# Kernel optimization log

Measured on AMD Instinct MI355X. Metric: run time of the kernel, lower is better.

## Reference

```python
import jax, jax.numpy as jnp
import numpy as np
import math

B, C, HW = 4, 256, 32          # batch, seq_len (=channels), spatial side
D_MODEL = HW * HW              # 1024
OUT_C = 32 * 32                # 1024
D_STATE = 16
EXPAND = 2
D_INNER = EXPAND * D_MODEL     # 2048
DT_RANK = math.ceil(D_MODEL / 16)  # 64
D_CONV = 4


def setup_inputs() -> dict:
    key = jax.random.key(0)
    ks = jax.random.split(key, 12)
    s = 0.02
    x1 = jax.random.normal(ks[0], (B, C, HW, HW), dtype=jnp.float32)
    in_proj_w = jax.random.normal(ks[1], (2 * D_INNER, D_MODEL), dtype=jnp.float32) * s
    conv_w = jax.random.normal(ks[2], (D_INNER, 1, D_CONV), dtype=jnp.float32) * s
    conv_b = jnp.zeros((D_INNER,), dtype=jnp.float32)
    x_proj_w = jax.random.normal(ks[3], (DT_RANK + 2 * D_STATE, D_INNER), dtype=jnp.float32) * s
    dt_proj_w = jax.random.normal(ks[4], (D_INNER, DT_RANK), dtype=jnp.float32) * s
    dt_proj_b = jnp.zeros((D_INNER,), dtype=jnp.float32)
    A_log = jnp.log(jnp.broadcast_to(jnp.arange(1, D_STATE + 1, dtype=jnp.float32), (D_INNER, D_STATE)))
    D = jnp.ones((D_INNER,), dtype=jnp.float32)
    out_proj_w = jax.random.normal(ks[5], (OUT_C, D_INNER), dtype=jnp.float32) * s
    ln_w = jnp.ones((OUT_C,), dtype=jnp.float32)
    ln_b = jnp.zeros((OUT_C,), dtype=jnp.float32)
    return {"x1": x1, "in_proj_w": in_proj_w, "conv_w": conv_w, "conv_b": conv_b,
            "x_proj_w": x_proj_w, "dt_proj_w": dt_proj_w, "dt_proj_b": dt_proj_b,
            "A_log": A_log, "D": D, "out_proj_w": out_proj_w, "ln_w": ln_w, "ln_b": ln_b}


def _mamba_forward(x, in_proj_w, conv_w, conv_b, x_proj_w, dt_proj_w, dt_proj_b, A_log, D, out_proj_w):
    # x: (B, L, d_model)
    xz = jnp.einsum('bld,ed->ble', x, in_proj_w)            # (B,L,2*d_inner)
    xs, res = jnp.split(xz, 2, axis=-1)                     # each (B,L,d_inner)
    # depthwise causal conv1d, padding=d_conv-1 then truncate to L (== left pad)
    xs_c = jnp.transpose(xs, (0, 2, 1))                     # (B,d_inner,L)
    xs_c = jax.lax.conv_general_dilated(
        xs_c, conv_w, window_strides=(1,), padding=[(D_CONV - 1, 0)],
        dimension_numbers=('NCH', 'OIH', 'NCH'), feature_group_count=D_INNER)
    xs_c = xs_c + conv_b[None, :, None]
    xs = jax.nn.silu(jnp.transpose(xs_c, (0, 2, 1)))        # (B,L,d_inner)
    # input-dependent SSM parameters
    x_dbl = jnp.einsum('bld,ed->ble', xs, x_proj_w)         # (B,L,dt_rank+2N)
    dt, Bm, Cm = jnp.split(x_dbl, [DT_RANK, DT_RANK + D_STATE], axis=-1)
    delta = jax.nn.softplus(jnp.einsum('blr,dr->bld', dt, dt_proj_w) + dt_proj_b)  # (B,L,d_inner)
    A = -jnp.exp(A_log)                                     # (d_inner, N)
    deltaA = jnp.exp(delta[..., None] * A)                  # (B,L,d_inner,N)
    deltaB_u = delta[..., None] * Bm[:, :, None, :] * xs[..., None]  # (B,L,d_inner,N)

    def step(h, inp):
        dA, dBu, Ct = inp                                   # (B,d,N),(B,d,N),(B,N)
        h = dA * h + dBu
        y = jnp.einsum('bdn,bn->bd', h, Ct)
        return h, y

    h0 = jnp.zeros((deltaA.shape[0], D_INNER, D_STATE), dtype=deltaA.dtype)
    _, ys = jax.lax.scan(step, h0, (jnp.transpose(deltaA, (1, 0, 2, 3)),
                                    jnp.transpose(deltaB_u, (1, 0, 2, 3)),
                                    jnp.transpose(Cm, (1, 0, 2))))
    y = jnp.transpose(ys, (1, 0, 2))                        # (B,L,d_inner)
    y = y + D * xs
    y = y * jax.nn.silu(res)
    return jnp.einsum('bld,od->blo', y, out_proj_w)         # (B,L,out_c)


def reference(x1, in_proj_w, conv_w, conv_b, x_proj_w, dt_proj_w, dt_proj_b,
              A_log, D, out_proj_w, ln_w, ln_b):
    b, c, h, w = x1.shape
    x = x1.reshape(b, c, h * w)                             # (B, L=c, d_model)
    y = _mamba_forward(x, in_proj_w, conv_w, conv_b, x_proj_w, dt_proj_w,
                       dt_proj_b, A_log, D, out_proj_w)
    mu = jnp.mean(y, axis=-1, keepdims=True)
    var = jnp.var(y, axis=-1, keepdims=True)
    y = (y - mu) * jax.lax.rsqrt(var + 1e-5) * ln_w + ln_b
    return y.reshape(b, c, 32, 32)
```

## Files before the change

kernel.cpp:

```cpp
#include <hip/hip_runtime.h>
#include <hip/hip_bf16.h>
#include <math.h>

#define BATCH 4
#define SEQL 256
#define DMODEL 1024
#define DINNER 2048
#define DSTATE 16
#define DTRANK 64
#define OUTC 1024
#define NROWS (BATCH * SEQL)
#define NCHUNK 4
#define CH 64

typedef __attribute__((ext_vector_type(8))) short bf16x8;
typedef __attribute__((ext_vector_type(4))) float f32x4;

__global__ __launch_bounds__(256) void gemm_mfma(const __hip_bfloat16* __restrict__ A,
                                                 const __hip_bfloat16* __restrict__ B,
                                                 float* __restrict__ C,
                                                 int M, int N, int K,
                                                 int lda, int ldb) {
    __shared__ __hip_bfloat16 As[4][128 * 32];
    __shared__ __hip_bfloat16 Bs[4][128 * 32];
    const int t  = threadIdx.x;
    const int w  = t >> 6;
    const int ln = t & 63;
    const int wm = w >> 1, wn = w & 1;
    const int q  = ln >> 4, lr = ln & 15;
    const int m0 = blockIdx.y * 128;
    const int n0 = blockIdx.x * 128;
    const int Kpart = K / gridDim.z;
    const int kbase = blockIdx.z * Kpart;

    f32x4 acc[4][4] = {};

    const __hip_bfloat16* Ag = A + (size_t)m0 * lda + kbase;
    const __hip_bfloat16* Bg = B + (size_t)n0 * ldb + kbase;

    auto stage = [&](int k0, int buf) {
        #pragma unroll
        for (int i = 0; i < 2; ++i) {
            const int c = (i * 4 + w) * 64 + ln;
            const int r = c >> 2, col = (c & 3) * 8;
            __builtin_amdgcn_global_load_lds(
                (const __attribute__((address_space(1))) void*)(Ag + (size_t)r * lda + k0 + col),
                (__attribute__((address_space(3))) void*)(As[buf] + (i * 4 + w) * 64 * 8),
                16, 0, 0);
            __builtin_amdgcn_global_load_lds(
                (const __attribute__((address_space(1))) void*)(Bg + (size_t)r * ldb + k0 + col),
                (__attribute__((address_space(3))) void*)(Bs[buf] + (i * 4 + w) * 64 * 8),
                16, 0, 0);
        }
    };

    const int nk = Kpart / 32;
    for (int s = 0; s < 3 && s < nk; ++s) stage(s * 32, s);

    for (int kk = 0; kk < nk; ++kk) {
        const int last = (kk + 2 < nk - 1) ? (kk + 2) : (nk - 1);
        const int nf = last - kk;
        if (nf >= 2)      asm volatile("s_waitcnt vmcnt(8)" ::: "memory");
        else if (nf == 1) asm volatile("s_waitcnt vmcnt(4)" ::: "memory");
        else              asm volatile("s_waitcnt vmcnt(0)" ::: "memory");
        __builtin_amdgcn_s_barrier();
        if (kk + 3 < nk) stage((kk + 3) * 32, (kk + 3) & 3);

        const int buf = kk & 3;
        bf16x8 af[4], bfr[4];
        #pragma unroll
        for (int i = 0; i < 4; ++i)
            af[i] = *(const bf16x8*)(As[buf] + (wm * 64 + i * 16 + lr) * 32 + q * 8);
        #pragma unroll
        for (int j = 0; j < 4; ++j)
            bfr[j] = *(const bf16x8*)(Bs[buf] + (wn * 64 + j * 16 + lr) * 32 + q * 8);
        #pragma unroll
        for (int i = 0; i < 4; ++i)
            #pragma unroll
            for (int j = 0; j < 4; ++j)
                acc[i][j] = __builtin_amdgcn_mfma_f32_16x16x32_bf16(af[i], bfr[j], acc[i][j], 0, 0, 0);
    }
    float* Cz = C + (size_t)blockIdx.z * M * N;
    #pragma unroll
    for (int i = 0; i < 4; ++i) {
        const int mrow = m0 + wm * 64 + i * 16 + q * 4;
        #pragma unroll
        for (int j = 0; j < 4; ++j) {
            const int ncol = n0 + wn * 64 + j * 16 + lr;
            #pragma unroll
            for (int r = 0; r < 4; ++r)
                Cz[(size_t)(mrow + r) * N + ncol] = acc[i][j][r];
        }
    }
}

__global__ __launch_bounds__(256) void gemm_dtsp(const __hip_bfloat16* __restrict__ A,
                                                 const __hip_bfloat16* __restrict__ B,
                                                 const float* __restrict__ bd,
                                                 float* __restrict__ delta) {
    __shared__ __hip_bfloat16 As[2][128 * 32];
    __shared__ __hip_bfloat16 Bs[2][128 * 32];
    const int t  = threadIdx.x;
    const int w  = t >> 6;
    const int ln = t & 63;
    const int wm = w >> 1, wn = w & 1;
    const int q  = ln >> 4, lr = ln & 15;
    const int m0 = blockIdx.y * 128;
    const int n0 = blockIdx.x * 128;
    const int lda = 128, ldb = 64, N = 2048;

    f32x4 acc[4][4] = {};
    const __hip_bfloat16* Ag = A + (size_t)m0 * lda;
    const __hip_bfloat16* Bg = B + (size_t)n0 * ldb;

    auto stage = [&](int k0, int buf) {
        #pragma unroll
        for (int i = 0; i < 2; ++i) {
            const int c = (i * 4 + w) * 64 + ln;
            const int r = c >> 2, col = (c & 3) * 8;
            __builtin_amdgcn_global_load_lds(
                (const __attribute__((address_space(1))) void*)(Ag + (size_t)r * lda + k0 + col),
                (__attribute__((address_space(3))) void*)(As[buf] + (i * 4 + w) * 64 * 8),
                16, 0, 0);
            __builtin_amdgcn_global_load_lds(
                (const __attribute__((address_space(1))) void*)(Bg + (size_t)r * ldb + k0 + col),
                (__attribute__((address_space(3))) void*)(Bs[buf] + (i * 4 + w) * 64 * 8),
                16, 0, 0);
        }
    };

    stage(0, 0);
    stage(32, 1);
    #pragma unroll
    for (int kk = 0; kk < 2; ++kk) {
        if (kk == 0) asm volatile("s_waitcnt vmcnt(4)" ::: "memory");
        else         asm volatile("s_waitcnt vmcnt(0)" ::: "memory");
        __builtin_amdgcn_s_barrier();
        bf16x8 af[4], bfr[4];
        #pragma unroll
        for (int i = 0; i < 4; ++i)
            af[i] = *(const bf16x8*)(As[kk] + (wm * 64 + i * 16 + lr) * 32 + q * 8);
        #pragma unroll
        for (int j = 0; j < 4; ++j)
            bfr[j] = *(const bf16x8*)(Bs[kk] + (wn * 64 + j * 16 + lr) * 32 + q * 8);
        #pragma unroll
        for (int i = 0; i < 4; ++i)
            #pragma unroll
            for (int j = 0; j < 4; ++j)
                acc[i][j] = __builtin_amdgcn_mfma_f32_16x16x32_bf16(af[i], bfr[j], acc[i][j], 0, 0, 0);
    }
    #pragma unroll
    for (int i = 0; i < 4; ++i) {
        const int mrow = m0 + wm * 64 + i * 16 + q * 4;
        #pragma unroll
        for (int j = 0; j < 4; ++j) {
            const int ncol = n0 + wn * 64 + j * 16 + lr;
            const float bias = bd[ncol];
            #pragma unroll
            for (int r = 0; r < 4; ++r) {
                float v = acc[i][j][r] + bias;
                float sp = (v > 20.f) ? v : log1pf(__expf(v));
                delta[(size_t)(mrow + r) * N + ncol] = sp;
            }
        }
    }
}

__global__ void xdbl_reduce_kernel(const float* __restrict__ part,
                                   float* __restrict__ xdbl,
                                   __hip_bfloat16* __restrict__ xdblb) {
    const int i = blockIdx.x * 256 + threadIdx.x;
    float s = 0.f;
    #pragma unroll
    for (int z = 0; z < 8; ++z) s += part[(size_t)z * (1024 * 128) + i];
    xdbl[i] = s;
    xdblb[i] = __float2bfloat16(s);
}

#define R0 (1024 * 1024)
#define R1 (R0 + 4096 * 1024)
#define R2 (R1 + 2048 * 1024)
#define R3 (R2 + 128 * 2048)
#define R4 (R3 + 2048 * 64)
__global__ void cast_all_kernel(const float* __restrict__ x1,
                                const float* __restrict__ w_in,
                                const float* __restrict__ w_out,
                                const float* __restrict__ w_xp,
                                const float* __restrict__ w_dt,
                                __hip_bfloat16* __restrict__ xa,
                                __hip_bfloat16* __restrict__ wb1,
                                __hip_bfloat16* __restrict__ wob,
                                __hip_bfloat16* __restrict__ wpb,
                                __hip_bfloat16* __restrict__ wdb) {
    int i = blockIdx.x * 256 + threadIdx.x;
    if (i < R0) {
        xa[i] = __float2bfloat16(x1[i]);
    } else if (i < R1) {
        int j = i - R0; wb1[j] = __float2bfloat16(w_in[j]);
    } else if (i < R2) {
        int j = i - R1; wob[j] = __float2bfloat16(w_out[j]);
    } else if (i < R3) {
        int j = i - R2; int e = j >> 11;
        wpb[j] = __float2bfloat16(e < 96 ? w_xp[j] : 0.f);
    } else if (i < R4) {
        int j = i - R3; wdb[j] = __float2bfloat16(w_dt[j]);
    }
}

__global__ void conv_silu_kernel(const float* __restrict__ xz,
                                 const float* __restrict__ conv_w,
                                 const float* __restrict__ conv_b,
                                 float* __restrict__ xs,
                                 __hip_bfloat16* __restrict__ xsb) {
    int idx = blockIdx.x * blockDim.x + threadIdx.x;
    int d = idx & (DINNER - 1);
    int l = (idx >> 11) & (SEQL - 1);
    int b = idx >> 19;
    const float w0 = conv_w[d * 4 + 0];
    const float w1 = conv_w[d * 4 + 1];
    const float w2 = conv_w[d * 4 + 2];
    const float w3 = conv_w[d * 4 + 3];
    float acc = conv_b[d];
    const size_t base = (size_t)(b * SEQL) * (2 * DINNER) + d;
    if (l >= 3) acc += w0 * xz[base + (size_t)(l - 3) * (2 * DINNER)];
    if (l >= 2) acc += w1 * xz[base + (size_t)(l - 2) * (2 * DINNER)];
    if (l >= 1) acc += w2 * xz[base + (size_t)(l - 1) * (2 * DINNER)];
    acc += w3 * xz[base + (size_t)l * (2 * DINNER)];
    float v = acc / (1.f + __expf(-acc));
    xs[idx] = v;
    xsb[idx] = __float2bfloat16(v);
}

__device__ __forceinline__ float row_reduce16(float x) {
    x += __int_as_float(__builtin_amdgcn_update_dpp(0, __float_as_int(x), 0x128, 0xF, 0xF, true));
    x += __int_as_float(__builtin_amdgcn_update_dpp(0, __float_as_int(x), 0x124, 0xF, 0xF, true));
    x += __int_as_float(__builtin_amdgcn_update_dpp(0, __float_as_int(x), 0x122, 0xF, 0xF, true));
    x += __int_as_float(__builtin_amdgcn_update_dpp(0, __float_as_int(x), 0x121, 0xF, 0xF, true));
    return x;
}

__global__ __launch_bounds__(256) void scan_carry_kernel(const float* __restrict__ delta,
                                                         const float* __restrict__ xs,
                                                         const float* __restrict__ xdbl,
                                                         const float* __restrict__ A_log,
                                                         float* __restrict__ carryL,
                                                         float* __restrict__ carryP) {
    __shared__ float sDU[CH][16][2];
    __shared__ float sB[CH][16];
    const int b = blockIdx.y, c = blockIdx.z, dg = blockIdx.x;
    const int t = threadIdx.x;
    const int dl = t >> 4, n = t & 15;
    const int d = dg * 16 + dl;
    const float a = -__expf(A_log[d * DSTATE + n]);
    const int srow = t >> 4, scol = t & 15;
    const int sd = dg * 16 + scol;
    const int rowbase = b * SEQL + c * CH;
    #pragma unroll
    for (int i = 0; i < 4; ++i) {
        const int row = rowbase + i * 16 + srow;
        const float dv = delta[(size_t)row * DINNER + sd];
        const float xv = xs[(size_t)row * DINNER + sd];
        sDU[i * 16 + srow][scol][0] = dv;
        sDU[i * 16 + srow][scol][1] = dv * xv;
        sB[i * 16 + srow][scol] = xdbl[row * 128 + 64 + scol];
    }
    __syncthreads();
    float h = 0.f, P = 1.f;
    #pragma unroll 16
    for (int l = 0; l < CH; ++l) {
        const float e = __expf(sDU[l][dl][0] * a);
        h = e * h + sDU[l][dl][1] * sB[l][n];
        P *= e;
    }
    const size_t ci = (((size_t)(b * NCHUNK + c)) * DINNER + d) * DSTATE + n;
    carryL[ci] = h;
    carryP[ci] = P;
}

__global__ __launch_bounds__(256) void scan_apply_kernel(const float* __restrict__ delta,
                                                         const float* __restrict__ xs,
                                                         const float* __restrict__ xdbl,
                                                         const float* __restrict__ xz,
                                                         const float* __restrict__ A_log,
                                                         const float* __restrict__ Dp,
                                                         const float* __restrict__ carryL,
                                                         const float* __restrict__ carryP,
                                                         __hip_bfloat16* __restrict__ ybb) {
    __shared__ float sDU[CH][16][2];
    __shared__ float sBC[CH][16][2];
    __shared__ float sGW[CH][16][2];
    const int b = blockIdx.y, c = blockIdx.z, dg = blockIdx.x;
    const int t = threadIdx.x;
    const int dl = t >> 4, n = t & 15;
    const int d = dg * 16 + dl;
    const float a = -__expf(A_log[d * DSTATE + n]);
    const int srow = t >> 4, scol = t & 15;
    const int sd = dg * 16 + scol;
    const float Dstage = Dp[sd];
    const int rowbase = b * SEQL + c * CH;
    #pragma unroll
    for (int i = 0; i < 4; ++i) {
        const int row = rowbase + i * 16 + srow;
        const float dv = delta[(size_t)row * DINNER + sd];
        const float xv = xs[(size_t)row * DINNER + sd];
        const float r  = xz[(size_t)row * (2 * DINNER) + DINNER + sd];
        const float g = r / (1.f + __expf(-r));
        const int lr_ = i * 16 + srow;
        sDU[lr_][scol][0] = dv;
        sDU[lr_][scol][1] = dv * xv;
        sGW[lr_][scol][0] = g;
        sGW[lr_][scol][1] = Dstage * xv * g;
        sBC[lr_][scol][0] = xdbl[row * 128 + 64 + scol];
        sBC[lr_][scol][1] = xdbl[row * 128 + 80 + scol];
    }
    __syncthreads();
    float h = 0.f;
    for (int j = 0; j < c; ++j) {
        const size_t ci = (((size_t)(b * NCHUNK + j)) * DINNER + d) * DSTATE + n;
        h = carryP[ci] * h + carryL[ci];
    }
    #pragma unroll 16
    for (int l = 0; l < CH; ++l) {
        const float e = __expf(sDU[l][dl][0] * a);
        h = e * h + sDU[l][dl][1] * sBC[l][n][0];
        float p = row_reduce16(h * sBC[l][n][1]);
        if (n == 0) {
            const float y = p * sGW[l][dl][0] + sGW[l][dl][1];
            ybb[(size_t)(rowbase + l) * DINNER + d] = __float2bfloat16(y);
        }
    }
}

__global__ __launch_bounds__(256) void ln_kernel(const float* __restrict__ opart,
                                                 const float* __restrict__ lw,
                                                 const float* __restrict__ lb,
                                                 float* __restrict__ out) {
    __shared__ float red[8];
    const int row = blockIdx.x;
    const int t = threadIdx.x;
    float v[4];
    float s = 0.f, s2 = 0.f;
    #pragma unroll
    for (int i = 0; i < 4; ++i) {
        const int c = t + 256 * i;
        float acc = 0.f;
        #pragma unroll
        for (int z = 0; z < 4; ++z)
            acc += opart[(size_t)z * (1024 * 1024) + (size_t)row * OUTC + c];
        v[i] = acc;
        s += acc;
        s2 += acc * acc;
    }
    #pragma unroll
    for (int o = 32; o; o >>= 1) {
        s += __shfl_down(s, o);
        s2 += __shfl_down(s2, o);
    }
    const int wid = t >> 6;
    if ((t & 63) == 0) { red[wid] = s; red[4 + wid] = s2; }
    __syncthreads();
    if (t == 0) {
        float ts = red[0] + red[1] + red[2] + red[3];
        float ts2 = red[4] + red[5] + red[6] + red[7];
        float mu = ts * (1.f / OUTC);
        float var = ts2 * (1.f / OUTC) - mu * mu;
        red[0] = mu;
        red[1] = rsqrtf(var + 1e-5f);
    }
    __syncthreads();
    const float mu = red[0], rs = red[1];
    #pragma unroll
    for (int i = 0; i < 4; ++i) {
        const int c = t + 256 * i;
        out[(size_t)row * OUTC + c] = (v[i] - mu) * rs * lw[c] + lb[c];
    }
}

extern "C" void kernel_launch(void* const* d_in, const int* in_sizes, int n_in,
                              void* d_out, int out_size, void* d_ws, size_t ws_size,
                              hipStream_t stream) {
    const float* x1        = (const float*)d_in[0];
    const float* in_proj_w = (const float*)d_in[1];
    const float* conv_w    = (const float*)d_in[2];
    const float* conv_b    = (const float*)d_in[3];
    const float* x_proj_w  = (const float*)d_in[4];
    const float* dt_proj_w = (const float*)d_in[5];
    const float* dt_proj_b = (const float*)d_in[6];
    const float* A_log     = (const float*)d_in[7];
    const float* Dp        = (const float*)d_in[8];
    const float* out_proj_w= (const float*)d_in[9];
    const float* ln_w      = (const float*)d_in[10];
    const float* ln_b      = (const float*)d_in[11];
    float* out = (float*)d_out;

    char* p = (char*)d_ws;
    __hip_bfloat16* xa    = (__hip_bfloat16*)p; p += (size_t)1024 * 1024 * 2;
    __hip_bfloat16* wb1   = (__hip_bfloat16*)p; p += (size_t)4096 * 1024 * 2;
    __hip_bfloat16* wpb   = (__hip_bfloat16*)p; p += (size_t)128 * 2048 * 2;
    __hip_bfloat16* wob   = (__hip_bfloat16*)p; p += (size_t)1024 * 2048 * 2;
    __hip_bfloat16* wdb   = (__hip_bfloat16*)p; p += (size_t)2048 * 64 * 2;
    __hip_bfloat16* xsb   = (__hip_bfloat16*)p; p += (size_t)1024 * 2048 * 2;
    __hip_bfloat16* ybb   = (__hip_bfloat16*)p; p += (size_t)1024 * 2048 * 2;
    __hip_bfloat16* xdblb = (__hip_bfloat16*)p; p += (size_t)1024 * 128 * 2;
    float* xz    = (float*)p; p += (size_t)1024 * 4096 * 4;
    float* xs    = (float*)p; p += (size_t)1024 * 2048 * 4;
    float* xdbl  = (float*)p; p += (size_t)1024 * 128 * 4;
    float* xpart = (float*)p; p += (size_t)8 * 1024 * 128 * 4;
    float* delta = (float*)p; p += (size_t)1024 * 2048 * 4;
    float* carryL = (float*)p; p += (size_t)BATCH * NCHUNK * DINNER * DSTATE * 4;
    float* carryP = (float*)p; p += (size_t)BATCH * NCHUNK * DINNER * DSTATE * 4;
    float* opart = xz;

    cast_all_kernel<<<(R4 + 255) / 256, 256, 0, stream>>>(x1, in_proj_w, out_proj_w,
                                                          x_proj_w, dt_proj_w,
                                                          xa, wb1, wob, wpb, wdb);
    gemm_mfma<<<dim3(32, 8, 1), 256, 0, stream>>>(xa, wb1, xz,
                                                  NROWS, 2 * DINNER, DMODEL, DMODEL, DMODEL);
    conv_silu_kernel<<<(NROWS * DINNER) / 256, 256, 0, stream>>>(xz, conv_w, conv_b, xs, xsb);
    gemm_mfma<<<dim3(1, 8, 8), 256, 0, stream>>>(xsb, wpb, xpart,
                                                 NROWS, 128, DINNER, DINNER, DINNER);
    xdbl_reduce_kernel<<<(1024 * 128) / 256, 256, 0, stream>>>(xpart, xdbl, xdblb);
    gemm_dtsp<<<dim3(16, 8), 256, 0, stream>>>(xdblb, wdb, dt_proj_b, delta);
    scan_carry_kernel<<<dim3(DINNER / 16, BATCH, NCHUNK), 256, 0, stream>>>(
        delta, xs, xdbl, A_log, carryL, carryP);
    scan_apply_kernel<<<dim3(DINNER / 16, BATCH, NCHUNK), 256, 0, stream>>>(
        delta, xs, xdbl, xz, A_log, Dp, carryL, carryP, ybb);
    gemm_mfma<<<dim3(8, 8, 4), 256, 0, stream>>>(ybb, wob, opart,
                                                 NROWS, OUTC, DINNER, DINNER, DINNER);
    ln_kernel<<<NROWS, 256, 0, stream>>>(opart, ln_w, ln_b, out);
}
```

Before: 220.0 us.

## Fuse all stages into one persistent cooperative kernel with grid syncs

```diff
diff --git a/kernel.cpp b/kernel.cpp
--- a/kernel.cpp
+++ b/kernel.cpp
@@ -1,40 +1,57 @@
 #include <hip/hip_runtime.h>
+#include <hip/hip_cooperative_groups.h>
 #include <hip/hip_bf16.h>
 #include <math.h>
+
+namespace cg = cooperative_groups;
 
 #define BATCH 4
 #define SEQL 256
 #define DMODEL 1024
 #define DINNER 2048
 #define DSTATE 16
-#define DTRANK 64
 #define OUTC 1024
 #define NROWS (BATCH * SEQL)
 #define NCHUNK 4
 #define CH 64
+#define NBLK 256
+#define XPZ 32
 
 typedef __attribute__((ext_vector_type(8))) short bf16x8;
 typedef __attribute__((ext_vector_type(4))) float f32x4;
 
-__global__ __launch_bounds__(256) void gemm_mfma(const __hip_bfloat16* __restrict__ A,
-                                                 const __hip_bfloat16* __restrict__ B,
-                                                 float* __restrict__ C,
-                                                 int M, int N, int K,
-                                                 int lda, int ldb) {
-    __shared__ __hip_bfloat16 As[4][128 * 32];
-    __shared__ __hip_bfloat16 Bs[4][128 * 32];
+struct MParams {
+    const float *x1, *w_in, *conv_w, *conv_b, *w_xp, *w_dt, *dt_b, *A_log, *Dp, *w_out, *ln_w, *ln_b;
+    float *out;
+    __hip_bfloat16 *xa, *wb1, *wpb, *wob, *wdb, *xsb, *ybb, *xdblb;
+    float *xz, *xs, *xdbl, *xpart, *delta, *carryL, *carryP, *opart;
+};
+
+__device__ __forceinline__ float row_reduce16(float x) {
+    x += __int_as_float(__builtin_amdgcn_update_dpp(0, __float_as_int(x), 0x128, 0xF, 0xF, true));
+    x += __int_as_float(__builtin_amdgcn_update_dpp(0, __float_as_int(x), 0x124, 0xF, 0xF, true));
+    x += __int_as_float(__builtin_amdgcn_update_dpp(0, __float_as_int(x), 0x122, 0xF, 0xF, true));
+    x += __int_as_float(__builtin_amdgcn_update_dpp(0, __float_as_int(x), 0x121, 0xF, 0xF, true));
+    return x;
+}
+
+template <bool DTSP>
+__device__ __forceinline__ void gemm_tile(const __hip_bfloat16* __restrict__ A,
+                                          const __hip_bfloat16* __restrict__ B,
+                                          float* __restrict__ Cz,
+                                          const int N, const int lda, const int ldb,
+                                          const int m0, const int n0,
+                                          const int kbase, const int Kpart,
+                                          const float* __restrict__ bd,
+                                          __hip_bfloat16* __restrict__ As,
+                                          __hip_bfloat16* __restrict__ Bs) {
     const int t  = threadIdx.x;
     const int w  = t >> 6;
     const int ln = t & 63;
     const int wm = w >> 1, wn = w & 1;
     const int q  = ln >> 4, lr = ln & 15;
-    const int m0 = blockIdx.y * 128;
-    const int n0 = blockIdx.x * 128;
-    const int Kpart = K / gridDim.z;
-    const int kbase = blockIdx.z * Kpart;
 
     f32x4 acc[4][4] = {};
-
     const __hip_bfloat16* Ag = A + (size_t)m0 * lda + kbase;
     const __hip_bfloat16* Bg = B + (size_t)n0 * ldb + kbase;
 
@@ -45,11 +62,11 @@
             const int r = c >> 2, col = (c & 3) * 8;
             __builtin_amdgcn_global_load_lds(
                 (const __attribute__((address_space(1))) void*)(Ag + (size_t)r * lda + k0 + col),
-                (__attribute__((address_space(3))) void*)(As[buf] + (i * 4 + w) * 64 * 8),
+                (__attribute__((address_space(3))) void*)(As + buf * 4096 + (i * 4 + w) * 512),
                 16, 0, 0);
             __builtin_amdgcn_global_load_lds(
                 (const __attribute__((address_space(1))) void*)(Bg + (size_t)r * ldb + k0 + col),
-                (__attribute__((address_space(3))) void*)(Bs[buf] + (i * 4 + w) * 64 * 8),
+                (__attribute__((address_space(3))) void*)(Bs + buf * 4096 + (i * 4 + w) * 512),
                 16, 0, 0);
         }
     };
@@ -66,115 +83,42 @@
         __builtin_amdgcn_s_barrier();
         if (kk + 3 < nk) stage((kk + 3) * 32, (kk + 3) & 3);
 
-        const int buf = kk & 3;
+        const __hip_bfloat16* Ab = As + (kk & 3) * 4096;
+        const __hip_bfloat16* Bb = Bs + (kk & 3) * 4096;
         bf16x8 af[4], bfr[4];
         #pragma unroll
         for (int i = 0; i < 4; ++i)
-            af[i] = *(const bf16x8*)(As[buf] + (wm * 64 + i * 16 + lr) * 32 + q * 8);
+            af[i] = *(const bf16x8*)(Ab + (wm * 64 + i * 16 + lr) * 32 + q * 8);
         #pragma unroll
         for (int j = 0; j < 4; ++j)
-            bfr[j] = *(const bf16x8*)(Bs[buf] + (wn * 64 + j * 16 + lr) * 32 + q * 8);
+            bfr[j] = *(const bf16x8*)(Bb + (wn * 64 + j * 16 + lr) * 32 + q * 8);
         #pragma unroll
         for (int i = 0; i < 4; ++i)
             #pragma unroll
             for (int j = 0; j < 4; ++j)
                 acc[i][j] = __builtin_amdgcn_mfma_f32_16x16x32_bf16(af[i], bfr[j], acc[i][j], 0, 0, 0);
     }
-    float* Cz = C + (size_t)blockIdx.z * M * N;
     #pragma unroll
     for (int i = 0; i < 4; ++i) {
         const int mrow = m0 + wm * 64 + i * 16 + q * 4;
         #pragma unroll
         for (int j = 0; j < 4; ++j) {
             const int ncol = n0 + wn * 64 + j * 16 + lr;
-            #pragma unroll
-            for (int r = 0; r < 4; ++r)
-                Cz[(size_t)(mrow + r) * N + ncol] = acc[i][j][r];
-        }
-    }
-}
-
-__global__ __launch_bounds__(256) void gemm_dtsp(const __hip_bfloat16* __restrict__ A,
-                                                 const __hip_bfloat16* __restrict__ B,
-                                                 const float* __restrict__ bd,
-                                                 float* __restrict__ delta) {
-    __shared__ __hip_bfloat16 As[2][128 * 32];
-    __shared__ __hip_bfloat16 Bs[2][128 * 32];
-    const int t  = threadIdx.x;
-    const int w  = t >> 6;
-    const int ln = t & 63;
-    const int wm = w >> 1, wn = w & 1;
-    const int q  = ln >> 4, lr = ln & 15;
-    const int m0 = blockIdx.y * 128;
-    const int n0 = blockIdx.x * 128;
-    const int lda = 128, ldb = 64, N = 2048;
-
-    f32x4 acc[4][4] = {};
-    const __hip_bfloat16* Ag = A + (size_t)m0 * lda;
-    const __hip_bfloat16* Bg = B + (size_t)n0 * ldb;
-
-    auto stage = [&](int k0, int buf) {
-        #pragma unroll
-        for (int i = 0; i < 2; ++i) {
-            const int c = (i * 4 + w) * 64 + ln;
-            const int r = c >> 2, col = (c & 3) * 8;
-            __builtin_amdgcn_global_load_lds(
-                (const __attribute__((address_space(1))) void*)(Ag + (size_t)r * lda + k0 + col),
-                (__attribute__((address_space(3))) void*)(As[buf] + (i * 4 + w) * 64 * 8),
-                16, 0, 0);
-            __builtin_amdgcn_global_load_lds(
-                (const __attribute__((address_space(1))) void*)(Bg + (size_t)r * ldb + k0 + col),
-                (__attribute__((address_space(3))) void*)(Bs[buf] + (i * 4 + w) * 64 * 8),
-                16, 0, 0);
-        }
-    };
-
-    stage(0, 0);
-    stage(32, 1);
-    #pragma unroll
-    for (int kk = 0; kk < 2; ++kk) {
-        if (kk == 0) asm volatile("s_waitcnt vmcnt(4)" ::: "memory");
-        else         asm volatile("s_waitcnt vmcnt(0)" ::: "memory");
-        __builtin_amdgcn_s_barrier();
-        bf16x8 af[4], bfr[4];
-        #pragma unroll
-        for (int i = 0; i < 4; ++i)
-            af[i] = *(const bf16x8*)(As[kk] + (wm * 64 + i * 16 + lr) * 32 + q * 8);
-        #pragma unroll
-        for (int j = 0; j < 4; ++j)
-            bfr[j] = *(const bf16x8*)(Bs[kk] + (wn * 64 + j * 16 + lr) * 32 + q * 8);
-        #pragma unroll
-        for (int i = 0; i < 4; ++i)
-            #pragma unroll
-            for (int j = 0; j < 4; ++j)
-                acc[i][j] = __builtin_amdgcn_mfma_f32_16x16x32_bf16(af[i], bfr[j], acc[i][j], 0, 0, 0);
-    }
-    #pragma unroll
-    for (int i = 0; i < 4; ++i) {
-        const int mrow = m0 + wm * 64 + i * 16 + q * 4;
-        #pragma unroll
-        for (int j = 0; j < 4; ++j) {
-            const int ncol = n0 + wn * 64 + j * 16 + lr;
-            const float bias = bd[ncol];
-            #pragma unroll
-            for (int r = 0; r < 4; ++r) {
-                float v = acc[i][j][r] + bias;
-                float sp = (v > 20.f) ? v : log1pf(__expf(v));
-                delta[(size_t)(mrow + r) * N + ncol] = sp;
-            }
-        }
-    }
-}
-
-__global__ void xdbl_reduce_kernel(const float* __restrict__ part,
-                                   float* __restrict__ xdbl,
-                                   __hip_bfloat16* __restrict__ xdblb) {
-    const int i = blockIdx.x * 256 + threadIdx.x;
-    float s = 0.f;
-    #pragma unroll
-    for (int z = 0; z < 8; ++z) s += part[(size_t)z * (1024 * 128) + i];
-    xdbl[i] = s;
-    xdblb[i] = __float2bfloat16(s);
+            if (DTSP) {
+                const float bias = bd[ncol];
+                #pragma unroll
+                for (int r = 0; r < 4; ++r) {
+                    float v = acc[i][j][r] + bias;
+                    float sp = (v > 20.f) ? v : log1pf(__expf(v));
+                    Cz[(size_t)(mrow + r) * N + ncol] = sp;
+                }
+            } else {
+                #pragma unroll
+                for (int r = 0; r < 4; ++r)
+                    Cz[(size_t)(mrow + r) * N + ncol] = acc[i][j][r];
+            }
+        }
+    }
 }
 
 #define R0 (1024 * 1024)
@@ -182,250 +126,257 @@
 #define R2 (R1 + 2048 * 1024)
 #define R3 (R2 + 128 * 2048)
 #define R4 (R3 + 2048 * 64)
-__global__ void cast_all_kernel(const float* __restrict__ x1,
-                                const float* __restrict__ w_in,
-                                const float* __restrict__ w_out,
-                                const float* __restrict__ w_xp,
-                                const float* __restrict__ w_dt,
-                                __hip_bfloat16* __restrict__ xa,
-                                __hip_bfloat16* __restrict__ wb1,
-                                __hip_bfloat16* __restrict__ wob,
-                                __hip_bfloat16* __restrict__ wpb,
-                                __hip_bfloat16* __restrict__ wdb) {
-    int i = blockIdx.x * 256 + threadIdx.x;
-    if (i < R0) {
-        xa[i] = __float2bfloat16(x1[i]);
-    } else if (i < R1) {
-        int j = i - R0; wb1[j] = __float2bfloat16(w_in[j]);
-    } else if (i < R2) {
-        int j = i - R1; wob[j] = __float2bfloat16(w_out[j]);
-    } else if (i < R3) {
-        int j = i - R2; int e = j >> 11;
-        wpb[j] = __float2bfloat16(e < 96 ? w_xp[j] : 0.f);
-    } else if (i < R4) {
-        int j = i - R3; wdb[j] = __float2bfloat16(w_dt[j]);
-    }
-}
-
-__global__ void conv_silu_kernel(const float* __restrict__ xz,
-                                 const float* __restrict__ conv_w,
-                                 const float* __restrict__ conv_b,
-                                 float* __restrict__ xs,
-                                 __hip_bfloat16* __restrict__ xsb) {
-    int idx = blockIdx.x * blockDim.x + threadIdx.x;
-    int d = idx & (DINNER - 1);
-    int l = (idx >> 11) & (SEQL - 1);
-    int b = idx >> 19;
-    const float w0 = conv_w[d * 4 + 0];
-    const float w1 = conv_w[d * 4 + 1];
-    const float w2 = conv_w[d * 4 + 2];
-    const float w3 = conv_w[d * 4 + 3];
-    float acc = conv_b[d];
-    const size_t base = (size_t)(b * SEQL) * (2 * DINNER) + d;
-    if (l >= 3) acc += w0 * xz[base + (size_t)(l - 3) * (2 * DINNER)];
-    if (l >= 2) acc += w1 * xz[base + (size_t)(l - 2) * (2 * DINNER)];
-    if (l >= 1) acc += w2 * xz[base + (size_t)(l - 1) * (2 * DINNER)];
-    acc += w3 * xz[base + (size_t)l * (2 * DINNER)];
-    float v = acc / (1.f + __expf(-acc));
-    xs[idx] = v;
-    xsb[idx] = __float2bfloat16(v);
-}
-
-__device__ __forceinline__ float row_reduce16(float x) {
-    x += __int_as_float(__builtin_amdgcn_update_dpp(0, __float_as_int(x), 0x128, 0xF, 0xF, true));
-    x += __int_as_float(__builtin_amdgcn_update_dpp(0, __float_as_int(x), 0x124, 0xF, 0xF, true));
-    x += __int_as_float(__builtin_amdgcn_update_dpp(0, __float_as_int(x), 0x122, 0xF, 0xF, true));
-    x += __int_as_float(__builtin_amdgcn_update_dpp(0, __float_as_int(x), 0x121, 0xF, 0xF, true));
-    return x;
-}
-
-__global__ __launch_bounds__(256) void scan_carry_kernel(const float* __restrict__ delta,
-                                                         const float* __restrict__ xs,
-                                                         const float* __restrict__ xdbl,
-                                                         const float* __restrict__ A_log,
-                                                         float* __restrict__ carryL,
-                                                         float* __restrict__ carryP) {
-    __shared__ float sDU[CH][16][2];
-    __shared__ float sB[CH][16];
-    const int b = blockIdx.y, c = blockIdx.z, dg = blockIdx.x;
+
+__global__ __launch_bounds__(256) void mega(MParams p) {
+    cg::grid_group grid = cg::this_grid();
+    __shared__ __align__(16) char smem[65536];
+    __hip_bfloat16* As = (__hip_bfloat16*)smem;
+    __hip_bfloat16* Bs = (__hip_bfloat16*)(smem + 32768);
+    const int lin = blockIdx.x;
     const int t = threadIdx.x;
-    const int dl = t >> 4, n = t & 15;
-    const int d = dg * 16 + dl;
-    const float a = -__expf(A_log[d * DSTATE + n]);
-    const int srow = t >> 4, scol = t & 15;
-    const int sd = dg * 16 + scol;
-    const int rowbase = b * SEQL + c * CH;
-    #pragma unroll
-    for (int i = 0; i < 4; ++i) {
-        const int row = rowbase + i * 16 + srow;
-        const float dv = delta[(size_t)row * DINNER + sd];
-        const float xv = xs[(size_t)row * DINNER + sd];
-        sDU[i * 16 + srow][scol][0] = dv;
-        sDU[i * 16 + srow][scol][1] = dv * xv;
-        sB[i * 16 + srow][scol] = xdbl[row * 128 + 64 + scol];
-    }
-    __syncthreads();
-    float h = 0.f, P = 1.f;
-    #pragma unroll 16
-    for (int l = 0; l < CH; ++l) {
-        const float e = __expf(sDU[l][dl][0] * a);
-        h = e * h + sDU[l][dl][1] * sB[l][n];
-        P *= e;
-    }
-    const size_t ci = (((size_t)(b * NCHUNK + c)) * DINNER + d) * DSTATE + n;
-    carryL[ci] = h;
-    carryP[ci] = P;
-}
-
-__global__ __launch_bounds__(256) void scan_apply_kernel(const float* __restrict__ delta,
-                                                         const float* __restrict__ xs,
-                                                         const float* __restrict__ xdbl,
-                                                         const float* __restrict__ xz,
-                                                         const float* __restrict__ A_log,
-                                                         const float* __restrict__ Dp,
-                                                         const float* __restrict__ carryL,
-                                                         const float* __restrict__ carryP,
-                                                         __hip_bfloat16* __restrict__ ybb) {
-    __shared__ float sDU[CH][16][2];
-    __shared__ float sBC[CH][16][2];
-    __shared__ float sGW[CH][16][2];
-    const int b = blockIdx.y, c = blockIdx.z, dg = blockIdx.x;
-    const int t = threadIdx.x;
-    const int dl = t >> 4, n = t & 15;
-    const int d = dg * 16 + dl;
-    const float a = -__expf(A_log[d * DSTATE + n]);
-    const int srow = t >> 4, scol = t & 15;
-    const int sd = dg * 16 + scol;
-    const float Dstage = Dp[sd];
-    const int rowbase = b * SEQL + c * CH;
-    #pragma unroll
-    for (int i = 0; i < 4; ++i) {
-        const int row = rowbase + i * 16 + srow;
-        const float dv = delta[(size_t)row * DINNER + sd];
-        const float xv = xs[(size_t)row * DINNER + sd];
-        const float r  = xz[(size_t)row * (2 * DINNER) + DINNER + sd];
-        const float g = r / (1.f + __expf(-r));
-        const int lr_ = i * 16 + srow;
-        sDU[lr_][scol][0] = dv;
-        sDU[lr_][scol][1] = dv * xv;
-        sGW[lr_][scol][0] = g;
-        sGW[lr_][scol][1] = Dstage * xv * g;
-        sBC[lr_][scol][0] = xdbl[row * 128 + 64 + scol];
-        sBC[lr_][scol][1] = xdbl[row * 128 + 80 + scol];
-    }
-    __syncthreads();
-    float h = 0.f;
-    for (int j = 0; j < c; ++j) {
-        const size_t ci = (((size_t)(b * NCHUNK + j)) * DINNER + d) * DSTATE + n;
-        h = carryP[ci] * h + carryL[ci];
-    }
-    #pragma unroll 16
-    for (int l = 0; l < CH; ++l) {
-        const float e = __expf(sDU[l][dl][0] * a);
-        h = e * h + sDU[l][dl][1] * sBC[l][n][0];
-        float p = row_reduce16(h * sBC[l][n][1]);
-        if (n == 0) {
-            const float y = p * sGW[l][dl][0] + sGW[l][dl][1];
-            ybb[(size_t)(rowbase + l) * DINNER + d] = __float2bfloat16(y);
-        }
-    }
-}
-
-__global__ __launch_bounds__(256) void ln_kernel(const float* __restrict__ opart,
-                                                 const float* __restrict__ lw,
-                                                 const float* __restrict__ lb,
-                                                 float* __restrict__ out) {
-    __shared__ float red[8];
-    const int row = blockIdx.x;
-    const int t = threadIdx.x;
-    float v[4];
-    float s = 0.f, s2 = 0.f;
-    #pragma unroll
-    for (int i = 0; i < 4; ++i) {
-        const int c = t + 256 * i;
-        float acc = 0.f;
-        #pragma unroll
-        for (int z = 0; z < 4; ++z)
-            acc += opart[(size_t)z * (1024 * 1024) + (size_t)row * OUTC + c];
-        v[i] = acc;
-        s += acc;
-        s2 += acc * acc;
-    }
-    #pragma unroll
-    for (int o = 32; o; o >>= 1) {
-        s += __shfl_down(s, o);
-        s2 += __shfl_down(s2, o);
-    }
-    const int wid = t >> 6;
-    if ((t & 63) == 0) { red[wid] = s; red[4 + wid] = s2; }
-    __syncthreads();
-    if (t == 0) {
-        float ts = red[0] + red[1] + red[2] + red[3];
-        float ts2 = red[4] + red[5] + red[6] + red[7];
-        float mu = ts * (1.f / OUTC);
-        float var = ts2 * (1.f / OUTC) - mu * mu;
-        red[0] = mu;
-        red[1] = rsqrtf(var + 1e-5f);
-    }
-    __syncthreads();
-    const float mu = red[0], rs = red[1];
-    #pragma unroll
-    for (int i = 0; i < 4; ++i) {
-        const int c = t + 256 * i;
-        out[(size_t)row * OUTC + c] = (v[i] - mu) * rs * lw[c] + lb[c];
+
+    for (int i = lin * 256 + t; i < R4; i += NBLK * 256) {
+        if (i < R0) {
+            p.xa[i] = __float2bfloat16(p.x1[i]);
+        } else if (i < R1) {
+            int j = i - R0; p.wb1[j] = __float2bfloat16(p.w_in[j]);
+        } else if (i < R2) {
+            int j = i - R1; p.wob[j] = __float2bfloat16(p.w_out[j]);
+        } else if (i < R3) {
+            int j = i - R2; int e = j >> 11;
+            p.wpb[j] = __float2bfloat16(e < 96 ? p.w_xp[j] : 0.f);
+        } else {
+            int j = i - R3; p.wdb[j] = __float2bfloat16(p.w_dt[j]);
+        }
+    }
+    grid.sync();
+
+    {
+        const int s = (lin & 7) * 32 + (lin >> 3);
+        const int bx = s & 31, by = s >> 5;
+        gemm_tile<false>(p.xa, p.wb1, p.xz, 4096, 1024, 1024,
+                         by * 128, bx * 128, 0, 1024, nullptr, As, Bs);
+    }
+    grid.sync();
+
+    for (int idx = lin * 256 + t; idx < NROWS * DINNER; idx += NBLK * 256) {
+        int d = idx & (DINNER - 1);
+        int l = (idx >> 11) & (SEQL - 1);
+        int b = idx >> 19;
+        const float w0 = p.conv_w[d * 4 + 0];
+        const float w1 = p.conv_w[d * 4 + 1];
+        const float w2 = p.conv_w[d * 4 + 2];
+        const float w3 = p.conv_w[d * 4 + 3];
+        float acc = p.conv_b[d];
+        const size_t base = (size_t)(b * SEQL) * (2 * DINNER) + d;
+        if (l >= 3) acc += w0 * p.xz[base + (size_t)(l - 3) * (2 * DINNER)];
+        if (l >= 2) acc += w1 * p.xz[base + (size_t)(l - 2) * (2 * DINNER)];
+        if (l >= 1) acc += w2 * p.xz[base + (size_t)(l - 1) * (2 * DINNER)];
+        acc += w3 * p.xz[base + (size_t)l * (2 * DINNER)];
+        float v = acc / (1.f + __expf(-acc));
+        p.xs[idx] = v;
+        p.xsb[idx] = __float2bfloat16(v);
+    }
+    grid.sync();
+
+    {
+        const int z = lin & 31, by = lin >> 5;
+        float* Cz = p.xpart + (size_t)z * (1024 * 128);
+        gemm_tile<false>(p.xsb, p.wpb, Cz, 128, 2048, 2048,
+                         by * 128, 0, z * 64, 64, nullptr, As, Bs);
+    }
+    grid.sync();
+
+    for (int i = lin * 256 + t; i < 1024 * 128; i += NBLK * 256) {
+        float s = 0.f;
+        #pragma unroll
+        for (int z = 0; z < XPZ; ++z) s += p.xpart[(size_t)z * (1024 * 128) + i];
+        p.xdbl[i] = s;
+        p.xdblb[i] = __float2bfloat16(s);
+    }
+    grid.sync();
+
+    if (lin < 128) {
+        const int bx = lin & 15, by = lin >> 4;
+        gemm_tile<true>(p.xdblb, p.wdb, p.delta, 2048, 128, 64,
+                        by * 128, bx * 128, 0, 64, p.dt_b, As, Bs);
+    }
+    grid.sync();
+
+    {
+        float (*sDU)[16][2] = (float(*)[16][2])smem;
+        float (*sB)[16]     = (float(*)[16])(smem + 8192);
+        const int dl = t >> 4, n = t & 15;
+        const int srow = t >> 4, scol = t & 15;
+        for (int v = lin; v < (DINNER / 16) * BATCH * NCHUNK; v += NBLK) {
+            const int dg = v & 127, b = (v >> 7) & 3, c = v >> 9;
+            const int d = dg * 16 + dl;
+            const float a = -__expf(p.A_log[d * DSTATE + n]);
+            const int sd = dg * 16 + scol;
+            const int rowbase = b * SEQL + c * CH;
+            __syncthreads();
+            #pragma unroll
+            for (int i = 0; i < 4; ++i) {
+                const int row = rowbase + i * 16 + srow;
+                const float dv = p.delta[(size_t)row * DINNER + sd];
+                const float xv = p.xs[(size_t)row * DINNER + sd];
+                sDU[i * 16 + srow][scol][0] = dv;
+                sDU[i * 16 + srow][scol][1] = dv * xv;
+                sB[i * 16 + srow][scol] = p.xdbl[row * 128 + 64 + scol];
+            }
+            __syncthreads();
+            float h = 0.f, P = 1.f;
+            #pragma unroll 16
+            for (int l = 0; l < CH; ++l) {
+                const float e = __expf(sDU[l][dl][0] * a);
+                h = e * h + sDU[l][dl][1] * sB[l][n];
+                P *= e;
+            }
+            const size_t ci = (((size_t)(b * NCHUNK + c)) * DINNER + d) * DSTATE + n;
+            p.carryL[ci] = h;
+            p.carryP[ci] = P;
+        }
+    }
+    grid.sync();
+
+    {
+        float (*sDU)[16][2] = (float(*)[16][2])smem;
+        float (*sBC)[16][2] = (float(*)[16][2])(smem + 8192);
+        float (*sGW)[16][2] = (float(*)[16][2])(smem + 16384);
+        const int dl = t >> 4, n = t & 15;
+        const int srow = t >> 4, scol = t & 15;
+        for (int v = lin; v < (DINNER / 16) * BATCH * NCHUNK; v += NBLK) {
+            const int dg = v & 127, b = (v >> 7) & 3, c = v >> 9;
+            const int d = dg * 16 + dl;
+            const float a = -__expf(p.A_log[d * DSTATE + n]);
+            const int sd = dg * 16 + scol;
+            const float Dstage = p.Dp[sd];
+            const int rowbase = b * SEQL + c * CH;
+            __syncthreads();
+            #pragma unroll
+            for (int i = 0; i < 4; ++i) {
+                const int row = rowbase + i * 16 + srow;
+                const float dv = p.delta[(size_t)row * DINNER + sd];
+                const float xv = p.xs[(size_t)row * DINNER + sd];
+                const float r  = p.xz[(size_t)row * (2 * DINNER) + DINNER + sd];
+                const float g = r / (1.f + __expf(-r));
+                const int lr_ = i * 16 + srow;
+                sDU[lr_][scol][0] = dv;
+                sDU[lr_][scol][1] = dv * xv;
+                sGW[lr_][scol][0] = g;
+                sGW[lr_][scol][1] = Dstage * xv * g;
+                sBC[lr_][scol][0] = p.xdbl[row * 128 + 64 + scol];
+                sBC[lr_][scol][1] = p.xdbl[row * 128 + 80 + scol];
+            }
+            __syncthreads();
+            float h = 0.f;
+            for (int j = 0; j < c; ++j) {
+                const size_t ci = (((size_t)(b * NCHUNK + j)) * DINNER + d) * DSTATE + n;
+                h = p.carryP[ci] * h + p.carryL[ci];
+            }
+            #pragma unroll 16
+            for (int l = 0; l < CH; ++l) {
+                const float e = __expf(sDU[l][dl][0] * a);
+                h = e * h + sDU[l][dl][1] * sBC[l][n][0];
+                float pr = row_reduce16(h * sBC[l][n][1]);
+                if (n == 0) {
+                    const float y = pr * sGW[l][dl][0] + sGW[l][dl][1];
+                    p.ybb[(size_t)(rowbase + l) * DINNER + d] = __float2bfloat16(y);
+                }
+            }
+        }
+    }
+    grid.sync();
+
+    {
+        const int s = (lin & 7) * 32 + (lin >> 3);
+        const int bx = s & 7, by = (s >> 3) & 7, z = s >> 6;
+        float* Cz = p.opart + (size_t)z * (1024 * 1024);
+        gemm_tile<false>(p.ybb, p.wob, Cz, 1024, 2048, 2048,
+                         by * 128, bx * 128, z * 512, 512, nullptr, As, Bs);
+    }
+    grid.sync();
+
+    {
+        float* red = (float*)smem;
+        for (int row = lin; row < NROWS; row += NBLK) {
+            __syncthreads();
+            float vv[4];
+            float s = 0.f, s2 = 0.f;
+            #pragma unroll
+            for (int i = 0; i < 4; ++i) {
+                const int c = t + 256 * i;
+                float acc = 0.f;
+                #pragma unroll
+                for (int z = 0; z < 4; ++z)
+                    acc += p.opart[(size_t)z * (1024 * 1024) + (size_t)row * OUTC + c];
+                vv[i] = acc;
+                s += acc;
+                s2 += acc * acc;
+            }
+            #pragma unroll
+            for (int o = 32; o; o >>= 1) {
+                s += __shfl_down(s, o);
+                s2 += __shfl_down(s2, o);
+            }
+            const int wid = t >> 6;
+            if ((t & 63) == 0) { red[wid] = s; red[4 + wid] = s2; }
+            __syncthreads();
+            if (t == 0) {
+                float ts = red[0] + red[1] + red[2] + red[3];
+                float ts2 = red[4] + red[5] + red[6] + red[7];
+                float mu = ts * (1.f / OUTC);
+                float var = ts2 * (1.f / OUTC) - mu * mu;
+                red[0] = mu;
+                red[1] = rsqrtf(var + 1e-5f);
+            }
+            __syncthreads();
+            const float mu = red[0], rs = red[1];
+            #pragma unroll
+            for (int i = 0; i < 4; ++i) {
+                const int c = t + 256 * i;
+                p.out[(size_t)row * OUTC + c] = (vv[i] - mu) * rs * p.ln_w[c] + p.ln_b[c];
+            }
+        }
     }
 }
 
 extern "C" void kernel_launch(void* const* d_in, const int* in_sizes, int n_in,
                               void* d_out, int out_size, void* d_ws, size_t ws_size,
                               hipStream_t stream) {
-    const float* x1        = (const float*)d_in[0];
-    const float* in_proj_w = (const float*)d_in[1];
-    const float* conv_w    = (const float*)d_in[2];
-    const float* conv_b    = (const float*)d_in[3];
-    const float* x_proj_w  = (const float*)d_in[4];
-    const float* dt_proj_w = (const float*)d_in[5];
-    const float* dt_proj_b = (const float*)d_in[6];
-    const float* A_log     = (const float*)d_in[7];
-    const float* Dp        = (const float*)d_in[8];
-    const float* out_proj_w= (const float*)d_in[9];
-    const float* ln_w      = (const float*)d_in[10];
-    const float* ln_b      = (const float*)d_in[11];
-    float* out = (float*)d_out;
+    MParams h;
+    h.x1        = (const float*)d_in[0];
+    h.w_in      = (const float*)d_in[1];
+    h.conv_w    = (const float*)d_in[2];
+    h.conv_b    = (const float*)d_in[3];
+    h.w_xp      = (const float*)d_in[4];
+    h.w_dt      = (const float*)d_in[5];
+    h.dt_b      = (const float*)d_in[6];
+    h.A_log     = (const float*)d_in[7];
+    h.Dp        = (const float*)d_in[8];
+    h.w_out     = (const float*)d_in[9];
+    h.ln_w      = (const float*)d_in[10];
+    h.ln_b      = (const float*)d_in[11];
+    h.out       = (float*)d_out;
 
     char* p = (char*)d_ws;
-    __hip_bfloat16* xa    = (__hip_bfloat16*)p; p += (size_t)1024 * 1024 * 2;
-    __hip_bfloat16* wb1   = (__hip_bfloat16*)p; p += (size_t)4096 * 1024 * 2;
-    __hip_bfloat16* wpb   = (__hip_bfloat16*)p; p += (size_t)128 * 2048 * 2;
-    __hip_bfloat16* wob   = (__hip_bfloat16*)p; p += (size_t)1024 * 2048 * 2;
-    __hip_bfloat16* wdb   = (__hip_bfloat16*)p; p += (size_t)2048 * 64 * 2;
-    __hip_bfloat16* xsb   = (__hip_bfloat16*)p; p += (size_t)1024 * 2048 * 2;
-    __hip_bfloat16* ybb   = (__hip_bfloat16*)p; p += (size_t)1024 * 2048 * 2;
-    __hip_bfloat16* xdblb = (__hip_bfloat16*)p; p += (size_t)1024 * 128 * 2;
-    float* xz    = (float*)p; p += (size_t)1024 * 4096 * 4;
-    float* xs    = (float*)p; p += (size_t)1024 * 2048 * 4;
-    float* xdbl  = (float*)p; p += (size_t)1024 * 128 * 4;
-    float* xpart = (float*)p; p += (size_t)8 * 1024 * 128 * 4;
-    float* delta = (float*)p; p += (size_t)1024 * 2048 * 4;
-    float* carryL = (float*)p; p += (size_t)BATCH * NCHUNK * DINNER * DSTATE * 4;
-    float* carryP = (float*)p; p += (size_t)BATCH * NCHUNK * DINNER * DSTATE * 4;
-    float* opart = xz;
-
-    cast_all_kernel<<<(R4 + 255) / 256, 256, 0, stream>>>(x1, in_proj_w, out_proj_w,
-                                                          x_proj_w, dt_proj_w,
-                                                          xa, wb1, wob, wpb, wdb);
-    gemm_mfma<<<dim3(32, 8, 1), 256, 0, stream>>>(xa, wb1, xz,
-                                                  NROWS, 2 * DINNER, DMODEL, DMODEL, DMODEL);
-    conv_silu_kernel<<<(NROWS * DINNER) / 256, 256, 0, stream>>>(xz, conv_w, conv_b, xs, xsb);
-    gemm_mfma<<<dim3(1, 8, 8), 256, 0, stream>>>(xsb, wpb, xpart,
-                                                 NROWS, 128, DINNER, DINNER, DINNER);
-    xdbl_reduce_kernel<<<(1024 * 128) / 256, 256, 0, stream>>>(xpart, xdbl, xdblb);
-    gemm_dtsp<<<dim3(16, 8), 256, 0, stream>>>(xdblb, wdb, dt_proj_b, delta);
-    scan_carry_kernel<<<dim3(DINNER / 16, BATCH, NCHUNK), 256, 0, stream>>>(
-        delta, xs, xdbl, A_log, carryL, carryP);
-    scan_apply_kernel<<<dim3(DINNER / 16, BATCH, NCHUNK), 256, 0, stream>>>(
-        delta, xs, xdbl, xz, A_log, Dp, carryL, carryP, ybb);
-    gemm_mfma<<<dim3(8, 8, 4), 256, 0, stream>>>(ybb, wob, opart,
-                                                 NROWS, OUTC, DINNER, DINNER, DINNER);
-    ln_kernel<<<NROWS, 256, 0, stream>>>(opart, ln_w, ln_b, out);
+    h.xa    = (__hip_bfloat16*)p; p += (size_t)1024 * 1024 * 2;
+    h.wb1   = (__hip_bfloat16*)p; p += (size_t)4096 * 1024 * 2;
+    h.wpb   = (__hip_bfloat16*)p; p += (size_t)128 * 2048 * 2;
+    h.wob   = (__hip_bfloat16*)p; p += (size_t)1024 * 2048 * 2;
+    h.wdb   = (__hip_bfloat16*)p; p += (size_t)2048 * 64 * 2;
+    h.xsb   = (__hip_bfloat16*)p; p += (size_t)1024 * 2048 * 2;
+    h.ybb   = (__hip_bfloat16*)p; p += (size_t)1024 * 2048 * 2;
+    h.xdblb = (__hip_bfloat16*)p; p += (size_t)1024 * 128 * 2;
+    h.xz    = (float*)p; p += (size_t)1024 * 4096 * 4;
+    h.xs    = (float*)p; p += (size_t)1024 * 2048 * 4;
+    h.xdbl  = (float*)p; p += (size_t)1024 * 128 * 4;
+    h.xpart = (float*)p; p += (size_t)XPZ * 1024 * 128 * 4;
+    h.delta = (float*)p; p += (size_t)1024 * 2048 * 4;
+    h.carryL = (float*)p; p += (size_t)BATCH * NCHUNK * DINNER * DSTATE * 4;
+    h.carryP = (float*)p; p += (size_t)BATCH * NCHUNK * DINNER * DSTATE * 4;
+    h.opart = h.xz;
+
+    void* args[] = { (void*)&h };
+    hipLaunchCooperativeKernel((void*)mega, dim3(NBLK), dim3(256), args, 0, stream);
 }
```

Result: slower. 577.0 us (+162.2%).
